# Optimization experiments

Hardware: AMD Instinct MI355X
Metric: run time of the kernel (lower is better)

The kernel has to match this reference:

```python
import jax, jax.numpy as jnp
import numpy as np
import math

B, T, D = 2, 2048, 1024
H = 16
d = D // H
I = 2816
RMS_EPS = 1e-6
GN_EPS = 1e-5


def setup_inputs() -> dict:
    key = jax.random.key(0)
    ks = jax.random.split(key, 12)
    s = 0.02
    gammas = 1.0 - jnp.exp(jnp.linspace(math.log(0.1), math.log(0.001), H)).astype(jnp.float32)
    return {
        "x": jax.random.normal(ks[0], (B, T, D), dtype=jnp.float32),
        "ln1_w": jnp.ones((D,), jnp.float32),
        "ln2_w": jnp.ones((D,), jnp.float32),
        "Wq": jax.random.normal(ks[1], (D, D), jnp.float32) * s,
        "Wk": jax.random.normal(ks[2], (D, D), jnp.float32) * s,
        "Wv": jax.random.normal(ks[3], (D, D), jnp.float32) * s,
        "Wg": jax.random.normal(ks[4], (D, D), jnp.float32) * s,
        "Wo": jax.random.normal(ks[5], (D, D), jnp.float32) * s,
        "gamma": gammas,
        "gn_w": jnp.ones((D,), jnp.float32),
        "gn_b": jnp.zeros((D,), jnp.float32),
        "gate_w": jax.random.normal(ks[6], (I, D), jnp.float32) * s,
        "up_w": jax.random.normal(ks[7], (I, D), jnp.float32) * s,
        "down_w": jax.random.normal(ks[8], (D, I), jnp.float32) * s,
    }


def _rmsnorm(x, w):
    var = jnp.mean(x * x, axis=-1, keepdims=True)
    return (x * jax.lax.rsqrt(var + RMS_EPS)) * w


def _retnet_scan(q, k, v, gamma):
    # q,k,v: (B,T,H,d); gamma: (H,)
    qT = jnp.moveaxis(q, 1, 0)  # (T,B,H,d)
    kT = jnp.moveaxis(k, 1, 0)
    vT = jnp.moveaxis(v, 1, 0)

    def step(S, qkv_t):
        q_t, k_t, v_t = qkv_t
        # S: (B,H,d,d) ; outer product k_t v_t^T
        S = gamma[None, :, None, None] * S + k_t[..., :, None] * v_t[..., None, :]
        o_t = jnp.einsum('bhd,bhde->bhe', q_t, S)
        return S, o_t

    S0 = jnp.zeros((q.shape[0], H, d, d), q.dtype)
    _, yT = jax.lax.scan(step, S0, (qT, kT, vT))  # yT: (T,B,H,d)
    return jnp.moveaxis(yT, 0, 1)  # (B,T,H,d)


def _group_norm(y, gn_w, gn_b):
    # y: (B,T,H,d). torch GroupNorm(H groups) on (B,D,T): normalize per (b, head)
    # over the (T, d) extent.
    mean = jnp.mean(y, axis=(1, 3), keepdims=True)
    var = jnp.var(y, axis=(1, 3), keepdims=True)
    yn = (y - mean) * jax.lax.rsqrt(var + GN_EPS)
    return yn * gn_w.reshape(1, 1, H, d) + gn_b.reshape(1, 1, H, d)


def reference(x, ln1_w, ln2_w, Wq, Wk, Wv, Wg, Wo, gamma, gn_w, gn_b, gate_w, up_w, down_w):
    Bx, Tx, Dx = x.shape
    h = _rmsnorm(x, ln1_w)
    q = (h @ Wq.T).reshape(Bx, Tx, H, d)
    k = (h @ Wk.T).reshape(Bx, Tx, H, d)
    v = (h @ Wv.T).reshape(Bx, Tx, H, d)
    g = jax.nn.sigmoid(h @ Wg.T)
    gam = jax.nn.sigmoid(gamma)
    y = _retnet_scan(q, k, v, gam)          # (B,T,H,d)
    y = _group_norm(y, gn_w, gn_b).reshape(Bx, Tx, Dx)
    y = g * y
    x = x + y @ Wo.T
    h2 = _rmsnorm(x, ln2_w)
    mlp = (jax.nn.silu(h2 @ gate_w.T) * (h2 @ up_w.T)) @ down_w.T
    return x + mlp
```

## Files before the change

### kernel.cpp

```cpp
#include <hip/hip_runtime.h>
#include <hip/hip_bf16.h>
#include <cstdint>
#include <cstddef>

typedef __bf16 bf16_t;
typedef __bf16 bf16x4 __attribute__((ext_vector_type(4)));
typedef __bf16 bf16x8 __attribute__((ext_vector_type(8)));
typedef float f32x4 __attribute__((ext_vector_type(4)));

#define DEVINL __device__ __forceinline__

#define TT 2048
#define DD 1024
#define HH 16
#define II 2816

DEVINL float waveSum(float v) {
#pragma unroll
  for (int m = 32; m >= 1; m >>= 1) v += __shfl_xor(v, m, 64);
  return v;
}

DEVINL float sigmoidf_(float z) { return 1.0f / (1.0f + __expf(-z)); }

DEVINL void gload_lds16(const bf16_t* g, bf16_t* l) {
  __builtin_amdgcn_global_load_lds((const __attribute__((address_space(1))) void*)g,
                                   (__attribute__((address_space(3))) void*)l, 16, 0, 0);
}

__global__ __launch_bounds__(256) void prep_kernel(const float* __restrict__ Wq,
                                                   const float* __restrict__ Wk,
                                                   const float* __restrict__ Wv,
                                                   const float* __restrict__ Wg,
                                                   const float* __restrict__ Wo,
                                                   const float* __restrict__ gate_w,
                                                   const float* __restrict__ up_w,
                                                   const float* __restrict__ down_w,
                                                   bf16_t* __restrict__ Wqkvg_bf,
                                                   bf16_t* __restrict__ Wo_bf,
                                                   bf16_t* __restrict__ GU_bf,
                                                   bf16_t* __restrict__ down_bf,
                                                   float* __restrict__ stats) {
  const int bid = blockIdx.x;
  const int tid = threadIdx.x;
  if (bid == 0 && tid < 64) stats[tid] = 0.f;
  if (bid < 5120) {
    const int which = bid >> 10;
    const float* src;
    bf16_t* dst;
    switch (which) {
      case 0: src = Wq; dst = Wqkvg_bf; break;
      case 1: src = Wk; dst = Wqkvg_bf + (size_t)DD * DD; break;
      case 2: src = Wv; dst = Wqkvg_bf + 2 * (size_t)DD * DD; break;
      case 3: src = Wg; dst = Wqkvg_bf + 3 * (size_t)DD * DD; break;
      default: src = Wo; dst = Wo_bf; break;
    }
    const int i = (bid & 1023) * 256 + tid;
    float4 v = reinterpret_cast<const float4*>(src)[i];
    bf16x4 o;
    o[0] = (bf16_t)v.x; o[1] = (bf16_t)v.y; o[2] = (bf16_t)v.z; o[3] = (bf16_t)v.w;
    reinterpret_cast<bf16x4*>(dst)[i] = o;
  } else if (bid < 10752) {
    const int r = bid - 5120;
    const int jb = r >> 5, s = r & 31;
    const float* src = (s < 16) ? (gate_w + (size_t)(jb * 16 + s) * DD)
                                : (up_w + (size_t)(jb * 16 + s - 16) * DD);
    float4 v = reinterpret_cast<const float4*>(src)[tid];
    bf16x4 o;
    o[0] = (bf16_t)v.x; o[1] = (bf16_t)v.y; o[2] = (bf16_t)v.z; o[3] = (bf16_t)v.w;
    reinterpret_cast<bf16x4*>(GU_bf + (size_t)r * DD)[tid] = o;
  } else {
    const int i = (bid - 10752) * 256 + tid;
    float4 v = reinterpret_cast<const float4*>(down_w)[i];
    bf16x4 o;
    o[0] = (bf16_t)v.x; o[1] = (bf16_t)v.y; o[2] = (bf16_t)v.z; o[3] = (bf16_t)v.w;
    reinterpret_cast<bf16x4*>(down_bf)[i] = o;
  }
}

__global__ __launch_bounds__(256) void rmsnorm_kernel(const float* __restrict__ x,
                                                      const float* __restrict__ w,
                                                      bf16_t* __restrict__ out) {
  const int row = blockIdx.x;
  const int tid = threadIdx.x;
  const float4 v = reinterpret_cast<const float4*>(x + (size_t)row * DD)[tid];
  float ss = v.x * v.x + v.y * v.y + v.z * v.z + v.w * v.w;
  ss = waveSum(ss);
  __shared__ float red[4];
  if ((tid & 63) == 0) red[tid >> 6] = ss;
  __syncthreads();
  const float total = red[0] + red[1] + red[2] + red[3];
  const float rstd = rsqrtf(total * (1.0f / (float)DD) + 1e-6f);
  const float4 wv = reinterpret_cast<const float4*>(w)[tid];
  bf16x4 o;
  o[0] = (bf16_t)(v.x * rstd * wv.x);
  o[1] = (bf16_t)(v.y * rstd * wv.y);
  o[2] = (bf16_t)(v.z * rstd * wv.z);
  o[3] = (bf16_t)(v.w * rstd * wv.w);
  reinterpret_cast<bf16x4*>(out + (size_t)row * DD)[tid] = o;
}

template <int EPI>
__global__ __launch_bounds__(512, 2) void gemm256(const bf16_t* __restrict__ A,
                                                  const bf16_t* __restrict__ B,
                                                  bf16_t* __restrict__ O1,
                                                  bf16_t* __restrict__ O2,
                                                  int M, int N, int K) {
  extern __shared__ __align__(16) char lds[];
  const int tid = threadIdx.x;
  const int wid = tid >> 6;
  const int lane = tid & 63;
  const int wr = wid >> 2;
  const int wc = wid & 3;
  const int row0 = blockIdx.y * 256;
  const int col0 = blockIdx.x * 256;

  const int s_row = wid * 8 + (lane >> 3);
  const int s_col = ((lane & 7) ^ (lane >> 3)) * 8;
  const bf16_t* gA = A + (size_t)(row0 + s_row) * K + s_col;
  const bf16_t* gB = B + (size_t)(col0 + s_row) * K + s_col;

  const int kq = lane >> 4;
  const int rl = lane & 15;
  const int xr = (lane & 7) << 4;

  f32x4 acc[8][4] = {};
  const int nt = K >> 6;

#pragma unroll
  for (int h = 0; h < 2; ++h)
#pragma unroll
    for (int ch = 0; ch < 2; ++ch) {
      gload_lds16(gA + (size_t)(h * 128 + ch * 64) * K,
                  (bf16_t*)(lds + h * 16384 + ch * 8192 + wid * 1024));
      gload_lds16(gB + (size_t)(h * 128 + ch * 64) * K,
                  (bf16_t*)(lds + 32768 + h * 16384 + ch * 8192 + wid * 1024));
    }
  asm volatile("s_waitcnt vmcnt(0)" ::: "memory");
  __builtin_amdgcn_s_barrier();

  for (int t = 0; t < nt; ++t) {
    const int cur = (t & 1) << 16;
    const int nxt = ((t + 1) & 1) << 16;
    const int k1 = (t + 1) << 6;
    const bool pf = (t + 1 < nt);
#pragma unroll
    for (int ph = 0; ph < 4; ++ph) {
      if (ph == 0 && pf) {
#pragma unroll
        for (int h = 0; h < 2; ++h)
#pragma unroll
          for (int ch = 0; ch < 2; ++ch)
            gload_lds16(gA + (size_t)(h * 128 + ch * 64) * K + k1,
                        (bf16_t*)(lds + nxt + h * 16384 + ch * 8192 + wid * 1024));
      }
      if (ph == 1 && pf) {
#pragma unroll
        for (int h = 0; h < 2; ++h)
#pragma unroll
          for (int ch = 0; ch < 2; ++ch)
            gload_lds16(gB + (size_t)(h * 128 + ch * 64) * K + k1,
                        (bf16_t*)(lds + nxt + 32768 + h * 16384 + ch * 8192 + wid * 1024));
      }
      const int mh = ph & 1, ks = ph >> 1;
      const int xk = (ks * 64 + kq * 16) ^ xr;
      const char* abase = lds + cur + wr * 16384;
      const char* bbase = lds + cur + 32768 + (wc >> 1) * 16384;
      bf16x8 aF[4], bF[4];
#pragma unroll
      for (int m = 0; m < 4; ++m) {
        const int ra = mh * 64 + m * 16 + rl;
        aF[m] = *reinterpret_cast<const bf16x8*>(abase + ra * 128 + xk);
      }
#pragma unroll
      for (int n = 0; n < 4; ++n) {
        const int rb = (wc & 1) * 64 + n * 16 + rl;
        bF[n] = *reinterpret_cast<const bf16x8*>(bbase + rb * 128 + xk);
      }
      __builtin_amdgcn_s_barrier();
      asm volatile("s_waitcnt lgkmcnt(0)" ::: "memory");
      __builtin_amdgcn_sched_barrier(0);
      __builtin_amdgcn_s_setprio(1);
#pragma unroll
      for (int m = 0; m < 4; ++m)
#pragma unroll
        for (int n = 0; n < 4; ++n)
          acc[mh * 4 + m][n] =
              __builtin_amdgcn_mfma_f32_16x16x32_bf16(aF[m], bF[n], acc[mh * 4 + m][n], 0, 0, 0);
      __builtin_amdgcn_s_setprio(0);
      if (ph == 3) asm volatile("s_waitcnt vmcnt(0)" ::: "memory");
      __builtin_amdgcn_s_barrier();
    }
  }

  const int crow = row0 + wr * 128 + kq * 4;
  const int ccol = col0 + wc * 64 + rl;
  if (EPI == 2) {
    const int obase = (col0 + wc * 64) / 2 + rl;
#pragma unroll
    for (int mf = 0; mf < 8; ++mf)
#pragma unroll
      for (int p = 0; p < 2; ++p)
#pragma unroll
        for (int r = 0; r < 4; ++r) {
          const float g = acc[mf][2 * p][r];
          const float u = acc[mf][2 * p + 1][r];
          O1[(size_t)(crow + mf * 16 + r) * II + (obase + p * 16)] =
              (bf16_t)(g * sigmoidf_(g) * u);
        }
  } else {
    if (col0 < 3072) {
#pragma unroll
      for (int mf = 0; mf < 8; ++mf)
#pragma unroll
        for (int n = 0; n < 4; ++n)
#pragma unroll
          for (int r = 0; r < 4; ++r)
            O1[(size_t)(crow + mf * 16 + r) * 3072 + (ccol + n * 16)] = (bf16_t)acc[mf][n][r];
    } else {
#pragma unroll
      for (int mf = 0; mf < 8; ++mf)
#pragma unroll
        for (int n = 0; n < 4; ++n)
#pragma unroll
          for (int r = 0; r < 4; ++r)
            O2[(size_t)(crow + mf * 16 + r) * DD + (ccol + n * 16 - 3072)] =
                (bf16_t)sigmoidf_(acc[mf][n][r]);
    }
  }
}

template <int EPI>
__global__ __launch_bounds__(256) void gemm_bt(const bf16_t* __restrict__ A,
                                               const bf16_t* __restrict__ B,
                                               float* __restrict__ C,
                                               const float* __restrict__ addsrc,
                                               int M, int N, int K) {
  __shared__ __align__(16) bf16_t smA[128 * 32];
  __shared__ __align__(16) bf16_t smB[128 * 32];
  const int tid = threadIdx.x;
  const int wid = tid >> 6;
  const int lane = tid & 63;
  const int row0 = blockIdx.y * 128;
  const int col0 = blockIdx.x * 128;
  const int wr = wid >> 1, wc = wid & 1;

  f32x4 acc[4][4] = {};

  const int sr = (wid * 2) * 16 + (lane >> 2);
  const int sc = (lane & 3) * 8;
  const bf16_t* gA = A + (size_t)(row0 + sr) * K + sc;
  const bf16_t* gB = B + (size_t)(col0 + sr) * K + sc;
  bf16_t* lA = smA + wid * 1024;
  bf16_t* lB = smB + wid * 1024;

  const int rl = lane & 15;
  const int kq = lane >> 4;
  const int aoff = (wr * 64 + rl) * 32 + kq * 8;
  const int boff = (wc * 64 + rl) * 32 + kq * 8;

  for (int k0 = 0; k0 < K; k0 += 32) {
#pragma unroll
    for (int j2 = 0; j2 < 2; ++j2) {
      gload_lds16(gA + (size_t)j2 * 16 * K + k0, lA + j2 * 512);
      gload_lds16(gB + (size_t)j2 * 16 * K + k0, lB + j2 * 512);
    }
    __syncthreads();
    bf16x8 aF[4], bF[4];
#pragma unroll
    for (int m = 0; m < 4; ++m)
      aF[m] = *reinterpret_cast<const bf16x8*>(smA + aoff + m * 16 * 32);
#pragma unroll
    for (int n = 0; n < 4; ++n)
      bF[n] = *reinterpret_cast<const bf16x8*>(smB + boff + n * 16 * 32);
#pragma unroll
    for (int m = 0; m < 4; ++m)
#pragma unroll
      for (int n = 0; n < 4; ++n)
        acc[m][n] = __builtin_amdgcn_mfma_f32_16x16x32_bf16(aF[m], bF[n], acc[m][n], 0, 0, 0);
    __syncthreads();
  }

  const int crow = row0 + wr * 64 + (lane >> 4) * 4;
  const int ccol = col0 + wc * 64 + rl;
#pragma unroll
  for (int m = 0; m < 4; ++m)
#pragma unroll
    for (int n = 0; n < 4; ++n)
#pragma unroll
      for (int r = 0; r < 4; ++r) {
        const size_t idx = (size_t)(crow + m * 16 + r) * N + (ccol + n * 16);
        float v = acc[m][n][r];
        if (EPI == 1) v += addsrc[idx];
        C[idx] = v;
      }
}

__global__ __launch_bounds__(256) void retscan_mfma(const bf16_t* __restrict__ qkv,
                                                    const float* __restrict__ gamma,
                                                    float* __restrict__ y,
                                                    float* __restrict__ stats) {
  const int c = blockIdx.x;
  const int bh = blockIdx.y;
  const int b = bh >> 4;
  const int h = bh & 15;
  const int tid = threadIdx.x;
  const int w = tid >> 6;
  const int lane = tid & 63;
  const int kq = lane >> 4;
  const int rl = lane & 15;

  __shared__ __align__(16) bf16_t K_lds[128 * 64];
  __shared__ __align__(16) bf16_t VT_lds[64 * 128];
  __shared__ __align__(16) bf16_t P_lds[64 * 128];
  __shared__ float rs[4][2];

  const size_t rstr = 3 * DD;
  const bf16_t* base = qkv + (size_t)(b * TT) * rstr + h * 64;
  const bf16_t* kgl = base + DD;
  const bf16_t* vgl = base + 2 * DD;

  for (int g = tid; g < 1024; g += 256) {
    const int sw = g >> 3, gr = g & 7;
    const int t = c * 64 - 64 + sw;
    bf16x8 kv = {};
    bf16x8 vv = {};
    if (t >= 0) {
      kv = *reinterpret_cast<const bf16x8*>(kgl + (size_t)t * rstr + gr * 8);
      vv = *reinterpret_cast<const bf16x8*>(vgl + (size_t)t * rstr + gr * 8);
    }
    *reinterpret_cast<bf16x8*>(K_lds + sw * 64 + ((gr ^ (sw & 7)) << 3)) = kv;
#pragma unroll
    for (int j = 0; j < 8; ++j) {
      const int e = gr * 8 + j;
      const int gs = (sw >> 3) ^ (e & 7);
      VT_lds[e * 128 + (gs << 3) + (sw & 7)] = vv[j];
    }
  }

  const int i0 = w * 16;
  const bf16_t* qrow = base + (size_t)(c * 64 + i0 + rl) * rstr;
  bf16x8 qF0 = *reinterpret_cast<const bf16x8*>(qrow + kq * 8);
  bf16x8 qF1 = *reinterpret_cast<const bf16x8*>(qrow + 32 + kq * 8);
  const float gam = sigmoidf_(gamma[h]);
  const float l2g = __log2f(gam);
  const float gi16 = exp2f(-16.f * l2g);

  __syncthreads();

  f32x4 S[8];
#pragma unroll
  for (int st = 0; st < 8; ++st) {
    const int sw = st * 16 + rl;
    const bf16_t* krow = K_lds + sw * 64;
    bf16x8 kF0 = *reinterpret_cast<const bf16x8*>(krow + ((kq ^ (sw & 7)) << 3));
    bf16x8 kF1 = *reinterpret_cast<const bf16x8*>(krow + (((4 + kq) ^ (sw & 7)) << 3));
    f32x4 s = {};
    s = __builtin_amdgcn_mfma_f32_16x16x32_bf16(qF0, kF0, s, 0, 0, 0);
    s = __builtin_amdgcn_mfma_f32_16x16x32_bf16(qF1, kF1, s, 0, 0, 0);
    S[st] = s;
  }

  float wgt[4];
  int lag[4];
#pragma unroll
  for (int r = 0; r < 4; ++r) {
    lag[r] = 64 + i0 + kq * 4 + r - rl;
    wgt[r] = exp2f((float)lag[r] * l2g);
  }
#pragma unroll
  for (int st = 0; st < 8; ++st) {
    const int sw = st * 16 + rl;
#pragma unroll
    for (int r = 0; r < 4; ++r) {
      const float p = (lag[r] >= 0) ? S[st][r] * wgt[r] : 0.f;
      const int i = i0 + kq * 4 + r;
      const int gs = (sw >> 3) ^ (i & 7);
      P_lds[i * 128 + (gs << 3) + (sw & 7)] = (bf16_t)p;
      lag[r] -= 16;
      wgt[r] *= gi16;
    }
  }
  asm volatile("s_waitcnt lgkmcnt(0)" ::: "memory");
  __builtin_amdgcn_sched_barrier(0);

  f32x4 Y[4] = {};
#pragma unroll
  for (int ks = 0; ks < 4; ++ks) {
    const int ia = i0 + rl;
    const int ga = (ks * 4 + kq) ^ (ia & 7);
    bf16x8 aF = *reinterpret_cast<const bf16x8*>(P_lds + ia * 128 + (ga << 3));
#pragma unroll
    for (int et = 0; et < 4; ++et) {
      const int e = et * 16 + rl;
      const int gb = (ks * 4 + kq) ^ (e & 7);
      bf16x8 bF = *reinterpret_cast<const bf16x8*>(VT_lds + e * 128 + (gb << 3));
      Y[et] = __builtin_amdgcn_mfma_f32_16x16x32_bf16(aF, bF, Y[et], 0, 0, 0);
    }
  }

  float s = 0.f, ss = 0.f;
  const size_t ybase = (size_t)(b * TT + c * 64 + i0 + kq * 4) * DD + h * 64 + rl;
#pragma unroll
  for (int et = 0; et < 4; ++et)
#pragma unroll
    for (int r = 0; r < 4; ++r) {
      const float v = Y[et][r];
      s += v;
      ss += v * v;
      y[ybase + (size_t)r * DD + et * 16] = v;
    }
  s = waveSum(s);
  ss = waveSum(ss);
  if (lane == 0) { rs[w][0] = s; rs[w][1] = ss; }
  __syncthreads();
  if (tid == 0) {
    atomicAdd(&stats[bh * 2], rs[0][0] + rs[1][0] + rs[2][0] + rs[3][0]);
    atomicAdd(&stats[bh * 2 + 1], rs[0][1] + rs[1][1] + rs[2][1] + rs[3][1]);
  }
}

__global__ __launch_bounds__(256) void gn_apply_kernel(const float* __restrict__ y,
                                                       const float* __restrict__ stats,
                                                       const bf16_t* __restrict__ gsig,
                                                       const float* __restrict__ gn_w,
                                                       const float* __restrict__ gn_b,
                                                       bf16_t* __restrict__ out) {
  const int row = blockIdx.x;
  const int tid = threadIdx.x;
  const int col = tid * 4;
  const int b = row >> 11;
  const int h = col >> 6;
  const float S = stats[(b * HH + h) * 2];
  const float SS = stats[(b * HH + h) * 2 + 1];
  const float inv = 1.0f / ((float)TT * 64.0f);
  const float mean = S * inv;
  const float var = SS * inv - mean * mean;
  const float rstd = rsqrtf(var + 1e-5f);
  float4 v = reinterpret_cast<const float4*>(y + (size_t)row * DD)[tid];
  float4 wv = reinterpret_cast<const float4*>(gn_w)[tid];
  float4 bv = reinterpret_cast<const float4*>(gn_b)[tid];
  bf16x4 gv = reinterpret_cast<const bf16x4*>(gsig + (size_t)row * DD)[tid];
  bf16x4 o;
  o[0] = (bf16_t)((((v.x - mean) * rstd) * wv.x + bv.x) * (float)gv[0]);
  o[1] = (bf16_t)((((v.y - mean) * rstd) * wv.y + bv.y) * (float)gv[1]);
  o[2] = (bf16_t)((((v.z - mean) * rstd) * wv.z + bv.z) * (float)gv[2]);
  o[3] = (bf16_t)((((v.w - mean) * rstd) * wv.w + bv.w) * (float)gv[3]);
  reinterpret_cast<bf16x4*>(out + (size_t)row * DD)[tid] = o;
}

extern "C" void kernel_launch(void* const* d_in, const int* in_sizes, int n_in,
                              void* d_out, int out_size, void* d_ws, size_t ws_size,
                              hipStream_t stream) {
  const float* x = (const float*)d_in[0];
  const float* ln1_w = (const float*)d_in[1];
  const float* ln2_w = (const float*)d_in[2];
  const float* Wq = (const float*)d_in[3];
  const float* Wk = (const float*)d_in[4];
  const float* Wv = (const float*)d_in[5];
  const float* Wg = (const float*)d_in[6];
  const float* Wo = (const float*)d_in[7];
  const float* gamma = (const float*)d_in[8];
  const float* gn_w = (const float*)d_in[9];
  const float* gn_b = (const float*)d_in[10];
  const float* gate_w = (const float*)d_in[11];
  const float* up_w = (const float*)d_in[12];
  const float* down_w = (const float*)d_in[13];
  float* out = (float*)d_out;

  const int M = 2 * TT;

  char* ws = (char*)d_ws;
  size_t off = 0;
  auto alloc = [&](size_t bytes) -> void* {
    void* p = ws + off;
    off += (bytes + 255) & ~(size_t)255;
    return p;
  };
  bf16_t* h_bf = (bf16_t*)alloc((size_t)M * DD * 2);
  bf16_t* Wqkvg_bf = (bf16_t*)alloc((size_t)4 * DD * DD * 2);
  bf16_t* Wo_bf = (bf16_t*)alloc((size_t)DD * DD * 2);
  bf16_t* GU_bf = (bf16_t*)alloc((size_t)2 * II * DD * 2);
  bf16_t* down_bf = (bf16_t*)alloc((size_t)DD * II * 2);
  bf16_t* qkv_bf = (bf16_t*)alloc((size_t)M * 3 * DD * 2);
  bf16_t* gsig = (bf16_t*)alloc((size_t)M * DD * 2);
  float* yBuf = (float*)alloc((size_t)M * DD * 4);
  bf16_t* ygated = (bf16_t*)alloc((size_t)M * DD * 2);
  bf16_t* act = (bf16_t*)alloc((size_t)M * II * 2);
  float* stats = (float*)alloc(64 * 4);
  (void)ws_size; (void)in_sizes; (void)n_in; (void)out_size;

  float* x2 = yBuf;

  prep_kernel<<<13568, 256, 0, stream>>>(Wq, Wk, Wv, Wg, Wo, gate_w, up_w, down_w,
                                         Wqkvg_bf, Wo_bf, GU_bf, down_bf, stats);

  rmsnorm_kernel<<<M, 256, 0, stream>>>(x, ln1_w, h_bf);

  {
    dim3 g(4 * DD / 256, M / 256);
    gemm256<3><<<g, 512, 131072, stream>>>(h_bf, Wqkvg_bf, qkv_bf, gsig, M, 4 * DD, DD);
  }

  {
    dim3 g(TT / 64, 2 * HH);
    retscan_mfma<<<g, 256, 0, stream>>>(qkv_bf, gamma, yBuf, stats);
  }

  gn_apply_kernel<<<M, 256, 0, stream>>>(yBuf, stats, gsig, gn_w, gn_b, ygated);

  {
    dim3 g(DD / 128, M / 128);
    gemm_bt<1><<<g, 256, 0, stream>>>(ygated, Wo_bf, x2, x, M, DD, DD);
  }

  rmsnorm_kernel<<<M, 256, 0, stream>>>(x2, ln2_w, h_bf);

  {
    dim3 g(2 * II / 256, M / 256);
    gemm256<2><<<g, 512, 131072, stream>>>(h_bf, GU_bf, act, nullptr, M, 2 * II, DD);
  }

  {
    dim3 g(DD / 128, M / 128);
    gemm_bt<1><<<g, 256, 0, stream>>>(act, down_bf, out, x2, M, DD, II);
  }
}
```

Baseline: 260.7 us.

## Switch GEMM mainloop to four-stage K=32 pipeline with XCD-aware block remap

After: 262.9 us. No clear change (+0.8%).

```diff
diff --git a/kernel.cpp b/kernel.cpp
--- a/kernel.cpp
+++ b/kernel.cpp
@@ -112,85 +112,69 @@
   const int lane = tid & 63;
   const int wr = wid >> 2;
   const int wc = wid & 3;
-  const int row0 = blockIdx.y * 256;
-  const int col0 = blockIdx.x * 256;
-
-  const int s_row = wid * 8 + (lane >> 3);
-  const int s_col = ((lane & 7) ^ (lane >> 3)) * 8;
+
+  const int gx = gridDim.x;
+  const int nwg = gx * gridDim.y;
+  int flat = blockIdx.y * gx + blockIdx.x;
+  flat = (flat & 7) * (nwg >> 3) + (flat >> 3);
+  const int row0 = (flat / gx) * 256;
+  const int col0 = (flat % gx) * 256;
+
+  const int s_row = wid * 32 + (lane >> 2);
+  const int s_col = (lane & 3) * 8;
   const bf16_t* gA = A + (size_t)(row0 + s_row) * K + s_col;
   const bf16_t* gB = B + (size_t)(col0 + s_row) * K + s_col;
 
   const int kq = lane >> 4;
   const int rl = lane & 15;
-  const int xr = (lane & 7) << 4;
 
   f32x4 acc[8][4] = {};
-  const int nt = K >> 6;
-
-#pragma unroll
-  for (int h = 0; h < 2; ++h)
-#pragma unroll
-    for (int ch = 0; ch < 2; ++ch) {
-      gload_lds16(gA + (size_t)(h * 128 + ch * 64) * K,
-                  (bf16_t*)(lds + h * 16384 + ch * 8192 + wid * 1024));
-      gload_lds16(gB + (size_t)(h * 128 + ch * 64) * K,
-                  (bf16_t*)(lds + 32768 + h * 16384 + ch * 8192 + wid * 1024));
-    }
-  asm volatile("s_waitcnt vmcnt(0)" ::: "memory");
+  const int nt = K >> 5;
+
+  auto stage = [&](int t) {
+    const int slot = (t & 3) * 32768;
+    const int ko = t << 5;
+#pragma unroll
+    for (int j = 0; j < 2; ++j) {
+      gload_lds16(gA + (size_t)j * 16 * K + ko,
+                  (bf16_t*)(lds + slot + wid * 2048 + j * 1024));
+      gload_lds16(gB + (size_t)j * 16 * K + ko,
+                  (bf16_t*)(lds + slot + 16384 + wid * 2048 + j * 1024));
+    }
+  };
+
+  stage(0); stage(1); stage(2);
+  asm volatile("s_waitcnt vmcnt(8)" ::: "memory");
   __builtin_amdgcn_s_barrier();
 
   for (int t = 0; t < nt; ++t) {
-    const int cur = (t & 1) << 16;
-    const int nxt = ((t + 1) & 1) << 16;
-    const int k1 = (t + 1) << 6;
-    const bool pf = (t + 1 < nt);
-#pragma unroll
-    for (int ph = 0; ph < 4; ++ph) {
-      if (ph == 0 && pf) {
-#pragma unroll
-        for (int h = 0; h < 2; ++h)
-#pragma unroll
-          for (int ch = 0; ch < 2; ++ch)
-            gload_lds16(gA + (size_t)(h * 128 + ch * 64) * K + k1,
-                        (bf16_t*)(lds + nxt + h * 16384 + ch * 8192 + wid * 1024));
-      }
-      if (ph == 1 && pf) {
-#pragma unroll
-        for (int h = 0; h < 2; ++h)
-#pragma unroll
-          for (int ch = 0; ch < 2; ++ch)
-            gload_lds16(gB + (size_t)(h * 128 + ch * 64) * K + k1,
-                        (bf16_t*)(lds + nxt + 32768 + h * 16384 + ch * 8192 + wid * 1024));
-      }
-      const int mh = ph & 1, ks = ph >> 1;
-      const int xk = (ks * 64 + kq * 16) ^ xr;
-      const char* abase = lds + cur + wr * 16384;
-      const char* bbase = lds + cur + 32768 + (wc >> 1) * 16384;
-      bf16x8 aF[4], bF[4];
-#pragma unroll
-      for (int m = 0; m < 4; ++m) {
-        const int ra = mh * 64 + m * 16 + rl;
-        aF[m] = *reinterpret_cast<const bf16x8*>(abase + ra * 128 + xk);
-      }
-#pragma unroll
-      for (int n = 0; n < 4; ++n) {
-        const int rb = (wc & 1) * 64 + n * 16 + rl;
-        bF[n] = *reinterpret_cast<const bf16x8*>(bbase + rb * 128 + xk);
-      }
-      __builtin_amdgcn_s_barrier();
-      asm volatile("s_waitcnt lgkmcnt(0)" ::: "memory");
-      __builtin_amdgcn_sched_barrier(0);
-      __builtin_amdgcn_s_setprio(1);
-#pragma unroll
-      for (int m = 0; m < 4; ++m)
-#pragma unroll
-        for (int n = 0; n < 4; ++n)
-          acc[mh * 4 + m][n] =
-              __builtin_amdgcn_mfma_f32_16x16x32_bf16(aF[m], bF[n], acc[mh * 4 + m][n], 0, 0, 0);
-      __builtin_amdgcn_s_setprio(0);
-      if (ph == 3) asm volatile("s_waitcnt vmcnt(0)" ::: "memory");
-      __builtin_amdgcn_s_barrier();
-    }
+    if (t + 4 <= nt) stage(t + 3);
+    const char* ab = lds + (t & 3) * 32768;
+    const char* bb = ab + 16384;
+    bf16x8 aF[8], bF[4];
+#pragma unroll
+    for (int m2 = 0; m2 < 8; ++m2)
+      aF[m2] = *reinterpret_cast<const bf16x8*>(ab + (wr * 128 + m2 * 16 + rl) * 64 + kq * 16);
+#pragma unroll
+    for (int n = 0; n < 4; ++n)
+      bF[n] = *reinterpret_cast<const bf16x8*>(bb + (wc * 64 + n * 16 + rl) * 64 + kq * 16);
+    asm volatile("s_waitcnt lgkmcnt(0)" ::: "memory");
+    __builtin_amdgcn_sched_barrier(0);
+    __builtin_amdgcn_s_setprio(1);
+#pragma unroll
+    for (int m2 = 0; m2 < 8; ++m2)
+#pragma unroll
+      for (int n = 0; n < 4; ++n)
+        acc[m2][n] = __builtin_amdgcn_mfma_f32_16x16x32_bf16(aF[m2], bF[n], acc[m2][n], 0, 0, 0);
+    __builtin_amdgcn_s_setprio(0);
+    if (t + 4 <= nt) {
+      asm volatile("s_waitcnt vmcnt(8)" ::: "memory");
+    } else if (t + 3 == nt) {
+      asm volatile("s_waitcnt vmcnt(4)" ::: "memory");
+    } else if (t + 2 == nt) {
+      asm volatile("s_waitcnt vmcnt(0)" ::: "memory");
+    }
+    __builtin_amdgcn_s_barrier();
   }
 
   const int crow = row0 + wr * 128 + kq * 4;
```
